# Kernel tuning notes

Hardware: AMD Instinct MI355X
Metric: run time of the kernel (lower is better)

Reference implementation:

```python
import jax, jax.numpy as jnp
import numpy as np

MAX_LENGTH = 25
SOS_TOKEN = 0


def setup_inputs() -> dict:
    key = jax.random.key(0)
    B, S, H, V = 32, 50, 256, 50257
    ks = jax.random.split(key, 16)
    u = lambda k, shape, fan: jax.random.uniform(k, shape, jnp.float32, -1.0, 1.0) / np.sqrt(fan)
    return {
        "encoder_hidden": jax.random.normal(ks[0], (1, B, H), jnp.float32),
        "encoder_outputs": jax.random.normal(ks[1], (B, S, H), jnp.float32),
        "target_tensor": jax.random.randint(ks[2], (B, MAX_LENGTH), 0, V),
        "embedding": jax.random.normal(ks[3], (V, H), jnp.float32) * 0.02,
        "Wa_w": u(ks[4], (H, H), H), "Wa_b": u(ks[5], (H,), H),
        "Ua_w": u(ks[6], (H, H), H), "Ua_b": u(ks[7], (H,), H),
        "Va_w": u(ks[8], (1, H), H), "Va_b": u(ks[9], (1,), H),
        "gru_w_ih": u(ks[10], (3 * H, 2 * H), H), "gru_b_ih": u(ks[11], (3 * H,), H),
        "gru_w_hh": u(ks[12], (3 * H, H), H), "gru_b_hh": u(ks[13], (3 * H,), H),
        "out_w": u(ks[14], (V, H), H), "out_b": u(ks[15], (V,), H),
    }


def reference(encoder_hidden, encoder_outputs, target_tensor, embedding,
              Wa_w, Wa_b, Ua_w, Ua_b, Va_w, Va_b,
              gru_w_ih, gru_b_ih, gru_w_hh, gru_b_hh, out_w, out_b):
    B, S, H = encoder_outputs.shape
    keys = encoder_outputs
    # Ua(keys) is step-invariant: precompute.  [B,S,H]
    ua_keys = jnp.einsum("bsh,gh->bsg", keys, Ua_w) + Ua_b
    # teacher-forced input tokens: [SOS, target[:, :-1]] -> [T,B]
    toks = jnp.concatenate(
        [jnp.full((B, 1), SOS_TOKEN, dtype=target_tensor.dtype),
         target_tensor[:, : MAX_LENGTH - 1]], axis=1).T

    def step(h, tok):
        # h: [B,H], tok: [B]
        emb = embedding[tok]                                   # [B,H]
        # Bahdanau attention (dropout is identity in eval mode)
        wa_q = h @ Wa_w.T + Wa_b                               # [B,H]
        e = jnp.tanh(wa_q[:, None, :] + ua_keys)               # [B,S,H]
        scores = jnp.einsum("bsh,h->bs", e, Va_w[0]) + Va_b[0]  # [B,S]
        w = jax.nn.softmax(scores, axis=-1)                    # [B,S]
        ctx = jnp.einsum("bs,bsh->bh", w, keys)                # [B,H]
        # GRU cell (PyTorch gate order: r, z, n)
        x = jnp.concatenate([emb, ctx], axis=-1)               # [B,2H]
        gi = x @ gru_w_ih.T + gru_b_ih                         # [B,3H]
        gh = h @ gru_w_hh.T + gru_b_hh                         # [B,3H]
        ir, iz, inn = jnp.split(gi, 3, axis=-1)
        hr, hz, hn = jnp.split(gh, 3, axis=-1)
        r = jax.nn.sigmoid(ir + hr)
        z = jax.nn.sigmoid(iz + hz)
        n = jnp.tanh(inn + r * hn)
        h2 = (1.0 - z) * n + z * h
        logits = h2 @ out_w.T + out_b                          # [B,V]
        return h2, (logits, w)

    h0 = encoder_hidden[0]                                     # [B,H]
    hT, (logits, attn) = jax.lax.scan(step, h0, toks)          # [T,B,V], [T,B,S]
    dec_out = jax.nn.log_softmax(logits.transpose(1, 0, 2), axis=-1)  # [B,T,V]
    attentions = attn.transpose(1, 0, 2)                       # [B,T,S]
    return dec_out, hT[None], attentions
```

## Files before the change

kernel.cpp:

```cpp
#include <hip/hip_runtime.h>
#include <math.h>

#define B_ 32
#define S_ 50
#define H_ 256
#define T_ 25
#define V_ 50257
#define VP 50264
#define NCH 786
#define NROW (B_ * T_)
#define NWROW 1024
#define VT_ 3144
#define MROW 54
#define SOS 0

typedef unsigned short ushort_t;
typedef __attribute__((ext_vector_type(8))) unsigned short ushort8;
typedef __attribute__((ext_vector_type(8))) short short8v;
typedef __attribute__((ext_vector_type(4))) float f32x4;
typedef _Float16 half2v __attribute__((ext_vector_type(2)));

__device__ ushort_t g_ua[B_ * S_ * H_];
__device__ ushort_t g_hbf[NROW * H_];
__device__ float    g_gie[T_ * B_ * 3 * H_];
__device__ ushort_t g_wpk[(size_t)VT_ * 32 * 16 * 8];
__device__ ushort_t g_wcat[NWROW * H_];
__device__ ushort_t g_MT2[B_ * 768 * MROW];
__device__ ushort_t g_lgt[(size_t)NROW * VP];
__device__ float    g_psum[NROW * NCH];

__device__ __forceinline__ float bf2f(ushort_t h) {
  union { unsigned int u; float f; } c; c.u = ((unsigned int)h) << 16; return c.f;
}
__device__ __forceinline__ ushort_t f2bf(float f) {
  union { float f; unsigned int u; } c; c.f = f;
  unsigned int u = c.u;
  return (ushort_t)((u + 0x7FFFu + ((u >> 16) & 1u)) >> 16);
}
__device__ __forceinline__ ushort_t f2h(float f) {
  union { _Float16 h; ushort_t u; } c; c.h = (_Float16)f; return c.u;
}
__device__ __forceinline__ float dot2(unsigned int a, unsigned int b, float c) {
#if __has_builtin(__builtin_amdgcn_fdot2)
  union { unsigned int u; half2v h; } ca, cb;
  ca.u = a; cb.u = b;
  return __builtin_amdgcn_fdot2(ca.h, cb.h, c, false);
#else
  union { unsigned int u; _Float16 h[2]; } ca, cb;
  ca.u = a; cb.u = b;
  return c + (float)ca.h[0] * (float)cb.h[0] + (float)ca.h[1] * (float)cb.h[1];
#endif
}
__device__ __forceinline__ float tanh_fast(float x) {
  const float e = __expf(2.f * x);
  return 1.f - 2.f / (e + 1.f);
}

__global__ void k_pre(const float* __restrict__ keys, const float* __restrict__ Ua_w,
                      const float* __restrict__ Ua_b, const float* __restrict__ Wa_b,
                      const float* __restrict__ W_hh, const float* __restrict__ Wa_w,
                      const float* __restrict__ W_ih, const float* __restrict__ b_ih,
                      const int* __restrict__ tgt, const float* __restrict__ emb_tab) {
  __shared__ float sbuf[16384];
  const int bid = blockIdx.x, tid = threadIdx.x;

  if (bid < 26) {
    ushort_t* sA = (ushort_t*)sbuf;
    const int bx = bid & 1, by = bid >> 1;
    const int n0 = bx * 128, m0 = by * 128;
    const int lane = tid & 63, wv = tid >> 6;
    const int wm = wv >> 1, wn = wv & 1;
    const int l16 = lane & 15, l4 = lane >> 4;

    for (int i = tid; i < 128 * 32; i += 256) {
      const int row = i >> 5, ks = i & 31;
      const int m = m0 + row;
      ushort8 val = {0, 0, 0, 0, 0, 0, 0, 0};
      if (m < B_ * S_) {
        const float4* kr = (const float4*)(keys + (size_t)m * H_ + ks * 8);
        const float4 f0 = kr[0], f1 = kr[1];
        val[0] = f2bf(f0.x); val[1] = f2bf(f0.y); val[2] = f2bf(f0.z); val[3] = f2bf(f0.w);
        val[4] = f2bf(f1.x); val[5] = f2bf(f1.y); val[6] = f2bf(f1.z); val[7] = f2bf(f1.w);
      }
      *(ushort8*)((char*)sA + row * 512 + ((ks ^ (row & 7)) << 4)) = val;
    }
    __syncthreads();

    f32x4 acc[4][4];
#pragma unroll
    for (int mi = 0; mi < 4; ++mi)
#pragma unroll
      for (int ni = 0; ni < 4; ++ni) acc[mi][ni] = (f32x4){0.f, 0.f, 0.f, 0.f};

#pragma unroll 1
    for (int kk = 0; kk < 8; ++kk) {
      short8v a[4], bfr[4];
#pragma unroll
      for (int mi = 0; mi < 4; ++mi) {
        const int row = wm * 64 + mi * 16 + l16;
        const int ks = kk * 4 + l4;
        a[mi] = *(const short8v*)((const char*)sA + row * 512 + ((ks ^ (row & 7)) << 4));
      }
#pragma unroll
      for (int ni = 0; ni < 4; ++ni) {
        const int g = n0 + wn * 64 + ni * 16 + l16;
        const float4* wr = (const float4*)(Ua_w + (size_t)g * H_ + kk * 32 + l4 * 8);
        const float4 f0 = wr[0], f1 = wr[1];
        short8v bv;
        bv[0] = (short)f2bf(f0.x); bv[1] = (short)f2bf(f0.y);
        bv[2] = (short)f2bf(f0.z); bv[3] = (short)f2bf(f0.w);
        bv[4] = (short)f2bf(f1.x); bv[5] = (short)f2bf(f1.y);
        bv[6] = (short)f2bf(f1.z); bv[7] = (short)f2bf(f1.w);
        bfr[ni] = bv;
      }
#pragma unroll
      for (int mi = 0; mi < 4; ++mi)
#pragma unroll
        for (int ni = 0; ni < 4; ++ni)
          acc[mi][ni] = __builtin_amdgcn_mfma_f32_16x16x32_bf16(a[mi], bfr[ni], acc[mi][ni], 0, 0, 0);
    }

    int col[4]; float bias[4];
#pragma unroll
    for (int ni = 0; ni < 4; ++ni) {
      col[ni] = n0 + wn * 64 + ni * 16 + l16;
      bias[ni] = Ua_b[col[ni]] + Wa_b[col[ni]];
    }
#pragma unroll
    for (int mi = 0; mi < 4; ++mi) {
#pragma unroll
      for (int j = 0; j < 4; ++j) {
        const int m = m0 + wm * 64 + mi * 16 + l4 * 4 + j;
        if (m < B_ * S_) {
#pragma unroll
          for (int ni = 0; ni < 4; ++ni)
            g_ua[(size_t)m * H_ + col[ni]] = f2bf(acc[mi][ni][j] + bias[ni]);
        }
      }
    }
  } else if (bid < 410) {
    const int cc = bid - 26;
    const int c = cc % 12, b = cc / 12;
    {
      const float4* src = (const float4*)(keys + (size_t)b * S_ * H_);
      float4* dst = (float4*)sbuf;
      for (int i = tid; i < S_ * H_ / 4; i += 256) dst[i] = src[i];
    }
    __syncthreads();
    const int sub = tid & 15, grp = tid >> 4;
#pragma unroll 1
    for (int it = 0; it < 4; ++it) {
      const int j = c * 64 + it * 16 + grp;
      float w16[16];
#pragma unroll
      for (int kp = 0; kp < 16; ++kp)
        w16[kp] = W_ih[(size_t)j * (2 * H_) + H_ + sub + 16 * kp];
#pragma unroll 1
      for (int s = 0; s < S_; ++s) {
        float a = 0.f;
#pragma unroll
        for (int kp = 0; kp < 16; ++kp) a += w16[kp] * sbuf[s * H_ + sub + 16 * kp];
        a += __shfl_xor(a, 8); a += __shfl_xor(a, 4);
        a += __shfl_xor(a, 2); a += __shfl_xor(a, 1);
        if (sub == 0) g_MT2[(size_t)b * 768 * MROW + j * MROW + s] = f2h(a);
      }
    }
  } else if (bid < 710) {
    const int cc = bid - 410;
    const int chunk = cc % 12, t = cc / 12;
    for (int i = tid; i < B_ * H_; i += 256) {
      const int b = i >> 8, g = i & 255;
      const int tok = (t == 0) ? SOS : tgt[b * T_ + (t - 1)];
      sbuf[i] = emb_tab[(size_t)tok * H_ + g];
    }
    __syncthreads();
    const int vl = tid & 63, wd = tid >> 6;
    const int j = chunk * 64 + vl;
    const float4* wrow = (const float4*)(W_ih + (size_t)j * (2 * H_));
    const float4* se4 = (const float4*)sbuf;
    float acc[8];
    const float base = b_ih[j];
#pragma unroll
    for (int bb = 0; bb < 8; ++bb) acc[bb] = base;
    for (int k4 = 0; k4 < 64; ++k4) {
      const float4 w = wrow[k4];
#pragma unroll
      for (int bb = 0; bb < 8; ++bb) {
        const float4 x = se4[(wd * 8 + bb) * 64 + k4];
        acc[bb] += w.x * x.x + w.y * x.y + w.z * x.z + w.w * x.w;
      }
    }
#pragma unroll
    for (int bb = 0; bb < 8; ++bb)
      g_gie[((size_t)t * B_ + (wd * 8 + bb)) * (3 * H_) + j] = acc[bb];
  } else {
    const size_t i0 = (size_t)(bid - 710) * 256 + tid;
    for (size_t i = i0; i < (size_t)NWROW * H_; i += 256u * 256u) {
      const int r = (int)(i >> 8), k = (int)(i & 255);
      const float v = (r < 256) ? Wa_w[r * H_ + k] : W_hh[(r - 256) * H_ + k];
      g_wcat[i] = f2h(v);
    }
  }
}

__global__ void __launch_bounds__(1024, 1)
k_recur(const float* __restrict__ enc_h, const float* __restrict__ Va_w,
        const float* __restrict__ Va_b, const float* __restrict__ b_hh,
        const float* __restrict__ out_w, float* __restrict__ out) {
  __shared__ ushort_t s_ua[S_ * H_];
  __shared__ ushort_t s_M[768 * MROW];
  __shared__ float s_res[NWROW];
  __shared__ float s_mw[768];
  __shared__ ushort_t s_hh[H_];
  __shared__ ushort_t s_wh[64];
  __shared__ float s_va[H_];
  __shared__ float s_score[64];
  const int bidx = blockIdx.x, tid = threadIdx.x;

  if (bidx >= 32) {
    const size_t total = (size_t)VT_ * 32 * 16;
    for (size_t p = (size_t)(bidx - 32) * 1024 + tid; p < total;
         p += (size_t)(gridDim.x - 32) * 1024) {
      const int c = (int)(p & 15);
      const int kg = (int)((p >> 4) & 31);
      const int vt = (int)(p >> 9);
      const int v = vt * 16 + c;
      short8v val = {0, 0, 0, 0, 0, 0, 0, 0};
      if (v < V_) {
        const float4* owr = (const float4*)(out_w + (size_t)v * H_ + kg * 8);
        const float4 f0 = owr[0], f1 = owr[1];
        val[0] = (short)f2bf(f0.x); val[1] = (short)f2bf(f0.y);
        val[2] = (short)f2bf(f0.z); val[3] = (short)f2bf(f0.w);
        val[4] = (short)f2bf(f1.x); val[5] = (short)f2bf(f1.y);
        val[6] = (short)f2bf(f1.z); val[7] = (short)f2bf(f1.w);
      }
      ((short8v*)g_wpk)[p] = val;
    }
    return;
  }

  const int b = bidx;
  const int lane = tid & 63, wid = tid >> 6;
  const int sub = lane & 15;
  const int grp = tid >> 4;

  {
    const uint4* src = (const uint4*)(g_ua + (size_t)b * S_ * H_);
    uint4* dst = (uint4*)s_ua;
    for (int i = tid; i < S_ * H_ / 8; i += 1024) dst[i] = src[i];
    const uint4* src2 = (const uint4*)(g_MT2 + (size_t)b * 768 * MROW);
    uint4* dst2 = (uint4*)s_M;
    for (int i = tid; i < 768 * MROW / 8; i += 1024) dst2[i] = src2[i];
  }
  float hreg = 0.f, bhh0 = 0.f, bhh1 = 0.f, bhh2 = 0.f;
  if (tid < H_) {
    hreg = enc_h[b * H_ + tid];
    s_hh[tid] = f2h(hreg);
    s_va[tid] = Va_w[tid];
    bhh0 = b_hh[tid]; bhh1 = b_hh[H_ + tid]; bhh2 = b_hh[2 * H_ + tid];
  }
  const float vab = Va_b[0];
  __syncthreads();

  for (int t = 0; t < T_; ++t) {
    float gie0 = 0.f, gie1 = 0.f, gie2 = 0.f;
    if (tid < H_) {
      const float* gp = g_gie + ((size_t)t * B_ + b) * (3 * H_);
      gie0 = gp[tid]; gie1 = gp[H_ + tid]; gie2 = gp[2 * H_ + tid];
    }

    {
      const unsigned int* hh = (const unsigned int*)s_hh;
#pragma unroll 4
      for (int it = 0; it < 16; ++it) {
        const int row = it * 64 + grp;
        const uint4* wr = (const uint4*)(g_wcat + (size_t)row * H_);
        const uint4 w0 = wr[sub], w1 = wr[16 + sub];
        float a = 0.f;
        a = dot2(w0.x, hh[sub * 4 + 0], a);
        a = dot2(w0.y, hh[sub * 4 + 1], a);
        a = dot2(w0.z, hh[sub * 4 + 2], a);
        a = dot2(w0.w, hh[sub * 4 + 3], a);
        a = dot2(w1.x, hh[64 + sub * 4 + 0], a);
        a = dot2(w1.y, hh[64 + sub * 4 + 1], a);
        a = dot2(w1.z, hh[64 + sub * 4 + 2], a);
        a = dot2(w1.w, hh[64 + sub * 4 + 3], a);
        a += __shfl_xor(a, 8); a += __shfl_xor(a, 4);
        a += __shfl_xor(a, 2); a += __shfl_xor(a, 1);
        if (sub == 0) s_res[row] = a;
      }
    }
    __syncthreads();

    for (int s = wid; s < S_; s += 16) {
      const ushort_t* uarow = s_ua + s * H_;
      float acc = 0.f;
#pragma unroll
      for (int i = 0; i < 4; ++i) {
        const int gg = lane + i * 64;
        acc += tanh_fast(s_res[gg] + bf2f(uarow[gg])) * s_va[gg];
      }
      for (int off = 32; off > 0; off >>= 1) acc += __shfl_xor(acc, off);
      if (lane == 0) s_score[s] = acc + vab;
    }
    __syncthreads();

    if (tid < 64) {
      const float v = (tid < S_) ? s_score[tid] : -INFINITY;
      float m = v;
      for (int off = 32; off > 0; off >>= 1) m = fmaxf(m, __shfl_xor(m, off));
      const float e = (tid < S_) ? __expf(v - m) : 0.f;
      float ssum = e;
      for (int off = 32; off > 0; off >>= 1) ssum += __shfl_xor(ssum, off);
      const float w = e / ssum;
      if (tid < S_) {
        s_wh[tid] = f2h(w);
        out[(size_t)B_ * T_ * V_ + (size_t)B_ * H_ + (size_t)(b * T_ + t) * S_ + tid] = w;
      }
    }
    __syncthreads();

    if (tid < 768) {
      const unsigned int* m32 = (const unsigned int*)s_M + tid * (MROW / 2);
      const unsigned int* ww = (const unsigned int*)s_wh;
      float acc = 0.f;
#pragma unroll
      for (int i = 0; i < 25; ++i) acc = dot2(m32[i], ww[i], acc);
      s_mw[tid] = acc;
    }
    __syncthreads();

    if (tid < H_) {
      const float gi0 = gie0 + s_mw[tid];
      const float gi1 = gie1 + s_mw[H_ + tid];
      const float gi2 = gie2 + s_mw[2 * H_ + tid];
      const float gh0 = s_res[256 + tid] + bhh0;
      const float gh1 = s_res[512 + tid] + bhh1;
      const float gh2 = s_res[768 + tid] + bhh2;
      const float r = 1.f / (1.f + __expf(-(gi0 + gh0)));
      const float z = 1.f / (1.f + __expf(-(gi1 + gh1)));
      const float n = tanh_fast(gi2 + r * gh2);
      const float h2 = (1.f - z) * n + z * hreg;
      hreg = h2;
      s_hh[tid] = f2h(h2);
      g_hbf[((size_t)b * T_ + t) * H_ + tid] = f2bf(h2);
      if (t == T_ - 1) out[(size_t)B_ * T_ * V_ + b * H_ + tid] = h2;
    }
    __syncthreads();
  }
}

__global__ void __launch_bounds__(512, 1)
k_logits(const float* __restrict__ out_b) {
  __shared__ ushort_t sA[128 * 256];
  __shared__ ushort_t sB[128 * 256];
  const int tid = threadIdx.x, nb = blockIdx.x;
  const int n0 = nb * 128;
  const int lane = tid & 63, wv = tid >> 6;
  const int wm = wv >> 1, wn = wv & 1;
  const int l16 = lane & 15, l4 = lane >> 4;

  {
    const short8v* src = (const short8v*)g_wpk + (size_t)nb * 4096;
    short8v* dst = (short8v*)sB;
    for (int i = tid; i < 4096; i += 512) dst[i] = src[i];
  }

  int vcol[4]; float bias[4]; bool valid[4];
#pragma unroll
  for (int ni = 0; ni < 4; ++ni) {
    vcol[ni] = n0 + wn * 64 + ni * 16 + l16;
    valid[ni] = (vcol[ni] < V_);
    bias[ni] = valid[ni] ? out_b[vcol[ni]] : 0.f;
  }
  const int chunk = nb * 2 + wn;

#pragma unroll 1
  for (int mt = 0; mt < 7; ++mt) {
    const int m0 = mt * 128;
    __syncthreads();
    for (int i = tid; i < 128 * 32; i += 512) {
      const int row = i >> 5, ks = i & 31;
      const int m = m0 + row;
      ushort8 val;
      if (m < NROW) val = ((const ushort8*)(g_hbf + (size_t)m * H_))[ks];
      else { ushort8 z = {0, 0, 0, 0, 0, 0, 0, 0}; val = z; }
      *(ushort8*)((char*)sA + row * 512 + ((ks ^ (row & 7)) << 4)) = val;
    }
    __syncthreads();

    f32x4 acc[2][4];
#pragma unroll
    for (int mi = 0; mi < 2; ++mi)
#pragma unroll
      for (int ni = 0; ni < 4; ++ni) acc[mi][ni] = (f32x4){0.f, 0.f, 0.f, 0.f};

#pragma unroll 1
    for (int kk = 0; kk < 8; ++kk) {
      short8v a[2], bfr[4];
#pragma unroll
      for (int mi = 0; mi < 2; ++mi) {
        const int row = wm * 32 + mi * 16 + l16;
        const int ks = kk * 4 + l4;
        a[mi] = *(const short8v*)((const char*)sA + row * 512 + ((ks ^ (row & 7)) << 4));
      }
#pragma unroll
      for (int ni = 0; ni < 4; ++ni)
        bfr[ni] = ((const short8v*)sB)[(((wn * 4 + ni) * 32) + kk * 4 + l4) * 16 + l16];
#pragma unroll
      for (int mi = 0; mi < 2; ++mi)
#pragma unroll
        for (int ni = 0; ni < 4; ++ni)
          acc[mi][ni] = __builtin_amdgcn_mfma_f32_16x16x32_bf16(a[mi], bfr[ni], acc[mi][ni], 0, 0, 0);
    }

#pragma unroll
    for (int mi = 0; mi < 2; ++mi) {
#pragma unroll
      for (int j = 0; j < 4; ++j) {
        const int m = m0 + wm * 32 + mi * 16 + l4 * 4 + j;
        float vv[4];
        float es = 0.f;
#pragma unroll
        for (int ni = 0; ni < 4; ++ni) {
          vv[ni] = acc[mi][ni][j] + bias[ni];
          if (valid[ni]) es += __expf(vv[ni]);
        }
        es += __shfl_xor(es, 1); es += __shfl_xor(es, 2);
        es += __shfl_xor(es, 4); es += __shfl_xor(es, 8);
        if (m < NROW) {
#pragma unroll
          for (int ni = 0; ni < 4; ++ni)
            if (valid[ni]) g_lgt[(size_t)m * VP + vcol[ni]] = f2bf(vv[ni]);
          if (l16 == 0) g_psum[(size_t)m * NCH + chunk] = es;
        }
      }
    }
  }
}

__global__ void k_wlse(float* __restrict__ out) {
  __shared__ float red[4];
  const int r = blockIdx.x;
  const int tid = threadIdx.x;
  float s = 0.f;
  for (int i = tid; i < NCH; i += 256) s += g_psum[(size_t)r * NCH + i];
  for (int off = 32; off > 0; off >>= 1) s += __shfl_xor(s, off);
  if ((tid & 63) == 0) red[tid >> 6] = s;
  __syncthreads();
  s = red[0] + red[1] + red[2] + red[3];
  float lse = logf(s);
  if (!isfinite(lse)) lse = 0.f;
  const size_t obase = (size_t)r * V_;
  const unsigned int* row32 = (const unsigned int*)(g_lgt + (size_t)r * VP);
#pragma unroll 1
  for (int i = tid; i < V_ / 2; i += 256) {
    const unsigned int u = row32[i];
    out[obase + 2 * i]     = bf2f((ushort_t)(u & 0xffffu)) - lse;
    out[obase + 2 * i + 1] = bf2f((ushort_t)(u >> 16)) - lse;
  }
  if (tid == 0)
    out[obase + V_ - 1] = bf2f(g_lgt[(size_t)r * VP + V_ - 1]) - lse;
}

extern "C" void kernel_launch(void* const* d_in, const int* in_sizes, int n_in,
                              void* d_out, int out_size, void* d_ws, size_t ws_size,
                              hipStream_t stream) {
  const float* enc_h  = (const float*)d_in[0];
  const float* keys   = (const float*)d_in[1];
  const int*   tgt    = (const int*)d_in[2];
  const float* emb    = (const float*)d_in[3];
  const float* Wa_w   = (const float*)d_in[4];
  const float* Wa_b   = (const float*)d_in[5];
  const float* Ua_w   = (const float*)d_in[6];
  const float* Ua_b   = (const float*)d_in[7];
  const float* Va_w   = (const float*)d_in[8];
  const float* Va_b   = (const float*)d_in[9];
  const float* W_ih   = (const float*)d_in[10];
  const float* b_ih   = (const float*)d_in[11];
  const float* W_hh   = (const float*)d_in[12];
  const float* b_hh   = (const float*)d_in[13];
  const float* out_w  = (const float*)d_in[14];
  const float* out_b  = (const float*)d_in[15];
  float* out = (float*)d_out;
  (void)d_ws; (void)ws_size;

  hipLaunchKernelGGL(k_pre, dim3(966), dim3(256), 0, stream,
                     keys, Ua_w, Ua_b, Wa_b, W_hh, Wa_w, W_ih, b_ih, tgt, emb);
  hipLaunchKernelGGL(k_recur, dim3(32 + 1792), dim3(1024), 0, stream,
                     enc_h, Va_w, Va_b, b_hh, out_w, out);
  hipLaunchKernelGGL(k_logits, dim3(393), dim3(512), 0, stream, out_b);
  hipLaunchKernelGGL(k_wlse, dim3(NROW), dim3(256), 0, stream, out);
}
```

Before: 444.5 us.

## Move exp-sum from logits epilogue into log-softmax kernel and fuse GRU matvec

The logits GEMM epilogue no longer computes per-chunk exp partial sums or writes them to a global partial-sum buffer. The log-softmax kernel now re-reads each bf16 logits row, sums exps itself, and then writes normalized outputs, using 512 threads per row instead of 256. In the recurrent kernel, the 768-thread attention-context matvec plus extra barrier is merged into the 256-thread GRU gate stage, with each thread computing three dot products. This trades an extra read of the logits row (mostly cache-resident) and more per-thread work for a lighter GEMM epilogue and one fewer sync per timestep.

```diff
diff --git a/kernel.cpp b/kernel.cpp
--- a/kernel.cpp
+++ b/kernel.cpp
@@ -7,7 +7,6 @@
 #define T_ 25
 #define V_ 50257
 #define VP 50264
-#define NCH 786
 #define NROW (B_ * T_)
 #define NWROW 1024
 #define VT_ 3144
@@ -27,7 +26,6 @@
 __device__ ushort_t g_wcat[NWROW * H_];
 __device__ ushort_t g_MT2[B_ * 768 * MROW];
 __device__ ushort_t g_lgt[(size_t)NROW * VP];
-__device__ float    g_psum[NROW * NCH];
 
 __device__ __forceinline__ float bf2f(ushort_t h) {
   union { unsigned int u; float f; } c; c.u = ((unsigned int)h) << 16; return c.f;
@@ -210,7 +208,6 @@
   __shared__ ushort_t s_ua[S_ * H_];
   __shared__ ushort_t s_M[768 * MROW];
   __shared__ float s_res[NWROW];
-  __shared__ float s_mw[768];
   __shared__ ushort_t s_hh[H_];
   __shared__ ushort_t s_wh[64];
   __shared__ float s_va[H_];
@@ -320,20 +317,22 @@
     }
     __syncthreads();
 
-    if (tid < 768) {
-      const unsigned int* m32 = (const unsigned int*)s_M + tid * (MROW / 2);
+    if (tid < H_) {
       const unsigned int* ww = (const unsigned int*)s_wh;
-      float acc = 0.f;
-#pragma unroll
-      for (int i = 0; i < 25; ++i) acc = dot2(m32[i], ww[i], acc);
-      s_mw[tid] = acc;
-    }
-    __syncthreads();
-
-    if (tid < H_) {
-      const float gi0 = gie0 + s_mw[tid];
-      const float gi1 = gie1 + s_mw[H_ + tid];
-      const float gi2 = gie2 + s_mw[2 * H_ + tid];
+      const unsigned int* m0p = (const unsigned int*)s_M + tid * (MROW / 2);
+      const unsigned int* m1p = (const unsigned int*)s_M + (H_ + tid) * (MROW / 2);
+      const unsigned int* m2p = (const unsigned int*)s_M + (2 * H_ + tid) * (MROW / 2);
+      float mw0 = 0.f, mw1 = 0.f, mw2 = 0.f;
+#pragma unroll
+      for (int i = 0; i < 25; ++i) {
+        const unsigned int w = ww[i];
+        mw0 = dot2(m0p[i], w, mw0);
+        mw1 = dot2(m1p[i], w, mw1);
+        mw2 = dot2(m2p[i], w, mw2);
+      }
+      const float gi0 = gie0 + mw0;
+      const float gi1 = gie1 + mw1;
+      const float gi2 = gie2 + mw2;
       const float gh0 = s_res[256 + tid] + bhh0;
       const float gh1 = s_res[512 + tid] + bhh1;
       const float gh2 = s_res[768 + tid] + bhh2;
@@ -373,7 +372,6 @@
     valid[ni] = (vcol[ni] < V_);
     bias[ni] = valid[ni] ? out_b[vcol[ni]] : 0.f;
   }
-  const int chunk = nb * 2 + wn;
 
 #pragma unroll 1
   for (int mt = 0; mt < 7; ++mt) {
@@ -419,42 +417,38 @@
 #pragma unroll
       for (int j = 0; j < 4; ++j) {
         const int m = m0 + wm * 32 + mi * 16 + l4 * 4 + j;
-        float vv[4];
-        float es = 0.f;
-#pragma unroll
-        for (int ni = 0; ni < 4; ++ni) {
-          vv[ni] = acc[mi][ni][j] + bias[ni];
-          if (valid[ni]) es += __expf(vv[ni]);
+        if (m < NROW) {
+#pragma unroll
+          for (int ni = 0; ni < 4; ++ni)
+            if (valid[ni]) g_lgt[(size_t)m * VP + vcol[ni]] = f2bf(acc[mi][ni][j] + bias[ni]);
         }
-        es += __shfl_xor(es, 1); es += __shfl_xor(es, 2);
-        es += __shfl_xor(es, 4); es += __shfl_xor(es, 8);
-        if (m < NROW) {
-#pragma unroll
-          for (int ni = 0; ni < 4; ++ni)
-            if (valid[ni]) g_lgt[(size_t)m * VP + vcol[ni]] = f2bf(vv[ni]);
-          if (l16 == 0) g_psum[(size_t)m * NCH + chunk] = es;
-        }
       }
     }
   }
 }
 
 __global__ void k_wlse(float* __restrict__ out) {
-  __shared__ float red[4];
+  __shared__ float red[8];
   const int r = blockIdx.x;
   const int tid = threadIdx.x;
+  const unsigned int* row32 = (const unsigned int*)(g_lgt + (size_t)r * VP);
   float s = 0.f;
-  for (int i = tid; i < NCH; i += 256) s += g_psum[(size_t)r * NCH + i];
+#pragma unroll 1
+  for (int i = tid; i < V_ / 2; i += 512) {
+    const unsigned int u = row32[i];
+    s += __expf(bf2f((ushort_t)(u & 0xffffu)));
+    s += __expf(bf2f((ushort_t)(u >> 16)));
+  }
+  if (tid == 0) s += __expf(bf2f(g_lgt[(size_t)r * VP + V_ - 1]));
   for (int off = 32; off > 0; off >>= 1) s += __shfl_xor(s, off);
   if ((tid & 63) == 0) red[tid >> 6] = s;
   __syncthreads();
-  s = red[0] + red[1] + red[2] + red[3];
+  s = red[0] + red[1] + red[2] + red[3] + red[4] + red[5] + red[6] + red[7];
   float lse = logf(s);
   if (!isfinite(lse)) lse = 0.f;
   const size_t obase = (size_t)r * V_;
-  const unsigned int* row32 = (const unsigned int*)(g_lgt + (size_t)r * VP);
-#pragma unroll 1
-  for (int i = tid; i < V_ / 2; i += 256) {
+#pragma unroll 1
+  for (int i = tid; i < V_ / 2; i += 512) {
     const unsigned int u = row32[i];
     out[obase + 2 * i]     = bf2f((ushort_t)(u & 0xffffu)) - lse;
     out[obase + 2 * i + 1] = bf2f((ushort_t)(u >> 16)) - lse;
@@ -490,5 +484,5 @@
   hipLaunchKernelGGL(k_recur, dim3(32 + 1792), dim3(1024), 0, stream,
                      enc_h, Va_w, Va_b, b_hh, out_w, out);
   hipLaunchKernelGGL(k_logits, dim3(393), dim3(512), 0, stream, out_b);
-  hipLaunchKernelGGL(k_wlse, dim3(NROW), dim3(256), 0, stream, out);
-}
+  hipLaunchKernelGGL(k_wlse, dim3(NROW), dim3(512), 0, stream, out);
+}
```

Measured after the change: 440.4 us. About the same (-0.9%).
